# Kernel tuning notes

Measured on AMD Instinct MI355X. Metric: run time of the kernel, lower is better.

Reference implementation:

```python
import jax, jax.numpy as jnp
import numpy as np

B = 32
N = 1024  # half_size == num_delays == num_wavelength
DELTA_TAU = 1.5e-15
W_CENTER = 1.175e15  # center_frequency / 2
PULSE_THRESHOLD = 0.01
PENALTY = 10.0
REAL_W = 1.0; IMAG_W = 1.0; INT_W = 1.0; PHASE_W = 1.0; FROG_W = 1.0
MSE_WSUM = REAL_W + IMAG_W + INT_W + PHASE_W

# Hilbert mask exactly as in the torch source (even N branch): H[N//2+1:]=2, H[N//2]=1
_Hm = np.zeros(N, dtype=np.float32)
_Hm[N // 2 + 1:] = 2.0
_Hm[N // 2] = 1.0
HILBERT_MASK = jnp.asarray(_Hm)

# precomputed circular-shift gather indices: shifted[m, j] = x[(j - delay[m]) mod N]
_delays = np.arange(-(N // 2), N // 2)
SHIFT_IDX = jnp.asarray((np.arange(N)[None, :] - _delays[:, None]) % N)  # [N, N] int
SHIFT_FACTOR = jnp.exp(-1j * jnp.asarray(2.0 * W_CENTER * DELTA_TAU * _delays, dtype=jnp.float32)).astype(jnp.complex64)  # [N]


def hilbert(x):  # x: [N] real -> [N] complex analytical signal
    xf = jnp.fft.fft(x)
    return jnp.fft.ifft(xf * HILBERT_MASK)


def shg_mat(a):  # a: [N] complex -> [N, N] complex SHG matrix (vectorized createSHGmat)
    shifted = a[SHIFT_IDX]                                  # [N, N] all circular shifts
    rows = a[None, :] * shifted * SHIFT_FACTOR[None, :]     # elementwise complex multiply
    f = jnp.fft.fft(jnp.fft.fftshift(rows, axes=-1), axis=-1)  # one batched FFT
    return DELTA_TAU * jnp.fft.fftshift(f, axes=-1)


def _first_last(mask):  # mask: [B, N] bool -> per-sample first/last significant index with fallback
    any_m = jnp.any(mask, axis=1)
    first = jnp.where(any_m, jnp.argmax(mask, axis=1), 0)
    last = jnp.where(any_m, N - 1 - jnp.argmax(mask[:, ::-1], axis=1), N - 1)
    return first, last


def setup_inputs() -> dict:
    key = jax.random.key(0)
    k1, k2, k3 = jax.random.split(key, 3)
    prediction = jax.random.normal(k1, (B, N), dtype=jnp.float32)
    label = jax.random.normal(k2, (B, 2 * N), dtype=jnp.float32)
    shg_matrix = jax.random.uniform(k3, (B, 1, N, N), dtype=jnp.float32)
    return {"prediction": prediction, "label": label, "shg_matrix": shg_matrix}


def reference(prediction, label, shg_matrix):
    pa = jax.vmap(hilbert)(prediction)          # [B, N] complex64
    pr, pi = pa.real, pa.imag
    lr, li = label[:, :N], label[:, N:]
    l_int = lr ** 2 + li ** 2
    p_int = pr ** 2 + pi ** 2
    l_ph = jnp.arctan2(li, lr)
    p_ph = jnp.arctan2(pi, pr)

    # ---- FROG error ----
    shg_pred = jnp.abs(jax.vmap(shg_mat)(pa)) ** 2              # [B, N, N]
    shg_pred = shg_pred / jnp.max(shg_pred, axis=(1, 2), keepdims=True)  # normalizeSHGmatrix
    t_ref = shg_matrix[:, 0]                                    # [B, N, N]
    sum1 = jnp.sum(shg_pred * t_ref, axis=(1, 2))
    sum2 = jnp.sum(t_ref * t_ref, axis=(1, 2))
    mu = sum1 / sum2
    r = jnp.sum(shg_pred - mu[:, None, None] * t_ref, axis=(1, 2)) ** 2
    norm = (N * N) * jnp.max(shg_pred, axis=(1, 2)) ** 2
    frog = jnp.where(r == 0.0, 0.0, jnp.sqrt(r / norm))         # [B]

    # ---- weighted masked MSE ----
    fr, lr_idx = _first_last(jnp.abs(lr) > PULSE_THRESHOLD)
    fi, li_idx = _first_last(jnp.abs(li) > PULSE_THRESHOLD)
    first = jnp.minimum(fr, fi)
    last = jnp.maximum(lr_idx, li_idx)
    ar = jnp.arange(N)[None, :]
    in_range = (ar >= first[:, None]) & (ar < last[:, None])    # [first:last] slice semantics
    phase_mask = in_range.astype(jnp.float32)
    pulse_mask = jnp.where(in_range, PENALTY, 1.0)

    mse_real = jnp.mean((pr - lr) ** 2 * pulse_mask, axis=1) * REAL_W
    mse_imag = jnp.mean((pi - li) ** 2 * pulse_mask, axis=1) * IMAG_W
    mse_int = jnp.mean((p_int - l_int) ** 2 * pulse_mask, axis=1) * INT_W
    mse_ph = jnp.mean((p_ph - l_ph) ** 2 * phase_mask, axis=1) * PHASE_W
    mse = (mse_real + mse_imag + mse_int + mse_ph) / MSE_WSUM

    return jnp.mean(mse + FROG_W * frog)
```

## Files before the change

### kernel.cpp

```cpp
#include <hip/hip_runtime.h>
#include <math.h>

#define N 1024
#define BATCH 32
#define NT 512
#define ROWS 4
#define RSTRIDE 1092
#define P16(i) ((i) + ((i) >> 4))
#define PADC(i) ((i) + ((i) >> 5))

#define WSYNC() asm volatile("s_waitcnt lgkmcnt(0)" ::: "memory")

typedef float2 cf;
__device__ __forceinline__ cf cadd(cf a, cf b){ return make_float2(a.x+b.x, a.y+b.y); }
__device__ __forceinline__ cf csub(cf a, cf b){ return make_float2(a.x-b.x, a.y-b.y); }
__device__ __forceinline__ cf cmul(cf a, cf b){ return make_float2(a.x*b.x - a.y*b.y, a.x*b.y + a.y*b.x); }

__device__ __forceinline__ cf twiddle(float jn){
    float s = __builtin_amdgcn_sinf(jn);
    float c = __builtin_amdgcn_cosf(jn);
    return make_float2(c, -s);
}

__device__ __forceinline__ int rev10(int m){
    int r = (int)(__brev((unsigned)m) >> 22);
    return ((r & 0x155) << 1) | ((r >> 1) & 0x155);
}

__device__ __forceinline__ void bfly(cf x0, cf x1, cf x2, cf x3,
                                     cf& y0, cf& y1, cf& y2, cf& y3){
    cf A = cadd(x0,x2), Bs = cadd(x1,x3);
    cf C = csub(x0,x2), D = csub(x1,x3);
    cf Dmi = make_float2(D.y, -D.x);
    y0 = cadd(A,Bs); y1 = cadd(C,Dmi); y2 = csub(A,Bs); y3 = csub(C,Dmi);
}

__device__ __forceinline__ void dif4p(cf* w, int base, int q, cf w1, cf w2, cf w3){
    cf x0 = w[P16(base)], x1 = w[P16(base+q)], x2 = w[P16(base+2*q)], x3 = w[P16(base+3*q)];
    cf y0, y1, y2, y3; bfly(x0,x1,x2,x3,y0,y1,y2,y3);
    w[P16(base)]     = y0;
    w[P16(base+q)]   = cmul(y1,w1);
    w[P16(base+2*q)] = cmul(y2,w2);
    w[P16(base+3*q)] = cmul(y3,w3);
}

__device__ __forceinline__ void dif4h(cf* w, int base, int q, float jn){
    cf x0 = w[PADC(base)], x1 = w[PADC(base+q)], x2 = w[PADC(base+2*q)], x3 = w[PADC(base+3*q)];
    cf y0, y1, y2, y3; bfly(x0,x1,x2,x3,y0,y1,y2,y3);
    cf w1 = twiddle(jn), w2 = cmul(w1,w1), w3 = cmul(w2,w1);
    w[PADC(base)]     = y0;
    w[PADC(base+q)]   = cmul(y1,w1);
    w[PADC(base+2*q)] = cmul(y2,w2);
    w[PADC(base+3*q)] = cmul(y3,w3);
}
template<int LOG2N>
__device__ __forceinline__ void dif_stage(cf* w, int t){
    const int n = 1 << LOG2N, q = n >> 2;
    int j = t & (q - 1);
    int base = ((t >> (LOG2N - 2)) << LOG2N) + j;
    dif4h(w, base, q, (float)j * (1.0f / (float)n));
}
template<int LOG2N>
__device__ __forceinline__ void dit_stage(cf* w, int t){
    const int n = 1 << LOG2N, q = n >> 2;
    int j = t & (q - 1);
    int base = ((t >> (LOG2N - 2)) << LOG2N) + j;
    cf x0 = w[PADC(base)], x1 = w[PADC(base+q)], x2 = w[PADC(base+2*q)], x3 = w[PADC(base+3*q)];
    cf w1 = twiddle((float)j * (1.0f / (float)n));
    cf w2 = cmul(w1,w1), w3 = cmul(w2,w1);
    x1 = cmul(x1,w1); x2 = cmul(x2,w2); x3 = cmul(x3,w3);
    cf y0, y1, y2, y3; bfly(x0,x1,x2,x3,y0,y1,y2,y3);
    w[PADC(base)] = y0; w[PADC(base+q)] = y1; w[PADC(base+2*q)] = y2; w[PADC(base+3*q)] = y3;
}

__global__ __launch_bounds__(256) void hilbert_k(const float* __restrict__ pred,
                                                 const float* __restrict__ label,
                                                 cf* __restrict__ a,
                                                 cf* __restrict__ ca,
                                                 float* __restrict__ mseJ) {
    __shared__ cf wk[1056];
    __shared__ float rbuf[4][4];
    __shared__ int ibuf[4][4];
    __shared__ int s_first, s_last;
    int t = threadIdx.x, b = blockIdx.x;
    for (int i = t; i < N; i += 256) wk[PADC(i)] = make_float2(pred[b * N + i], 0.f);
    __syncthreads();
    dif_stage<10>(wk, t); __syncthreads();
    dif_stage<8>(wk, t);  __syncthreads();
    dif_stage<6>(wk, t);  __syncthreads();
    dif_stage<4>(wk, t);  __syncthreads();
    dif_stage<2>(wk, t);  __syncthreads();
    for (int i = t; i < N; i += 256) {
        int k = rev10(i);
        float f = (k < 512) ? 0.f : ((k == 512) ? 1.f : 2.f);
        cf v = wk[PADC(i)];
        wk[PADC(i)] = make_float2(f * v.x, -f * v.y);
    }
    __syncthreads();
    dit_stage<2>(wk, t);  __syncthreads();
    dit_stage<4>(wk, t);  __syncthreads();
    dit_stage<6>(wk, t);  __syncthreads();
    dit_stage<8>(wk, t);  __syncthreads();
    dit_stage<10>(wk, t); __syncthreads();
    const float sc = 1.f / (float)N;
    for (int i = t; i < N; i += 256) {
        cf v = wk[PADC(i)];
        cf av = make_float2(v.x * sc, -v.y * sc);
        wk[PADC(i)] = av;
        a[b * N + i] = av;
        float p = (float)(3.525 * (double)(i - 512));
        float s_, c_;
        sincosf(p, &s_, &c_);
        ca[b * N + i] = make_float2(av.x * c_ + av.y * s_, av.y * c_ - av.x * s_);
    }
    __syncthreads();

    int w = t >> 6, lane = t & 63;
    int mnR = N, mxR = -1, mnI = N, mxI = -1;
    for (int n = t; n < N; n += 256) {
        float lr = label[b * 2 * N + n];
        float li = label[b * 2 * N + N + n];
        if (fabsf(lr) > 0.01f) { mnR = min(mnR, n); mxR = max(mxR, n); }
        if (fabsf(li) > 0.01f) { mnI = min(mnI, n); mxI = max(mxI, n); }
    }
    for (int o = 32; o > 0; o >>= 1) {
        mnR = min(mnR, __shfl_down(mnR, o));
        mxR = max(mxR, __shfl_down(mxR, o));
        mnI = min(mnI, __shfl_down(mnI, o));
        mxI = max(mxI, __shfl_down(mxI, o));
    }
    if (lane == 0) { ibuf[w][0] = mnR; ibuf[w][1] = mxR; ibuf[w][2] = mnI; ibuf[w][3] = mxI; }
    __syncthreads();
    if (t == 0) {
        int a0 = N, a1 = -1, a2 = N, a3 = -1;
        for (int i = 0; i < 4; ++i) {
            a0 = min(a0, ibuf[i][0]); a1 = max(a1, ibuf[i][1]);
            a2 = min(a2, ibuf[i][2]); a3 = max(a3, ibuf[i][3]);
        }
        int fr   = (a0 == N) ? 0 : a0;
        int lstR = (a1 < 0) ? (N - 1) : a1;
        int fi   = (a2 == N) ? 0 : a2;
        int lstI = (a3 < 0) ? (N - 1) : a3;
        s_first = min(fr, fi);
        s_last  = max(lstR, lstI);
    }
    __syncthreads();
    int first = s_first, last = s_last;

    float m_r = 0.f, m_i = 0.f, m_n = 0.f, m_p = 0.f;
    for (int n = t; n < N; n += 256) {
        cf p = wk[PADC(n)];
        float lr = label[b * 2 * N + n];
        float li = label[b * 2 * N + N + n];
        bool in = (n >= first) && (n < last);
        float pm  = in ? 10.f : 1.f;
        float phm = in ? 1.f : 0.f;
        float dr = p.x - lr, di = p.y - li;
        float dn = (p.x * p.x + p.y * p.y) - (lr * lr + li * li);
        float dp = atan2f(p.y, p.x) - atan2f(li, lr);
        m_r += dr * dr * pm;
        m_i += di * di * pm;
        m_n += dn * dn * pm;
        m_p += dp * dp * phm;
    }
    for (int o = 32; o > 0; o >>= 1) {
        m_r += __shfl_down(m_r, o);
        m_i += __shfl_down(m_i, o);
        m_n += __shfl_down(m_n, o);
        m_p += __shfl_down(m_p, o);
    }
    if (lane == 0) { rbuf[w][0] = m_r; rbuf[w][1] = m_i; rbuf[w][2] = m_n; rbuf[w][3] = m_p; }
    __syncthreads();
    if (t == 0) {
        float s = 0.f;
        for (int i = 0; i < 4; ++i) s += rbuf[i][0] + rbuf[i][1] + rbuf[i][2] + rbuf[i][3];
        mseJ[b] = s * (1.f / (float)N) * 0.25f;
    }
}

__global__ __launch_bounds__(NT, 8) void shg_k(const cf* __restrict__ a,
                                               const cf* __restrict__ cag,
                                               const float* __restrict__ tref,
                                               float* __restrict__ Praw,
                                               float* __restrict__ Prt,
                                               float* __restrict__ Pmax,
                                               float* __restrict__ Pt,
                                               float* __restrict__ Ptt) {
    __shared__ cf wk[ROWS * RSTRIDE];
    int t = threadIdx.x, blk = blockIdx.x;
    int b = blk >> 8;
    int dg = (blk & 255) << 2;
    const cf* arow  = a   + b * N;
    const cf* carow = cag + b * N;
    int bt = t & 255, rg = t >> 8;

    {
        cf w1 = twiddle((float)bt * (1.0f / 1024.0f));
        cf w2 = cmul(w1,w1), w3 = cmul(w2,w1);
        cf cav[4];
#pragma unroll
        for (int k = 0; k < 4; ++k) cav[k] = carow[(bt + 256*k + 512) & 1023];
#pragma unroll
        for (int rr = 0; rr < 2; ++rr) {
            int r = rg * 2 + rr;
            int d = dg + r;
            cf x[4];
#pragma unroll
            for (int k = 0; k < 4; ++k)
                x[k] = cmul(cav[k], arow[(bt + 256*k - d) & 1023]);
            cf y0, y1, y2, y3; bfly(x[0],x[1],x[2],x[3],y0,y1,y2,y3);
            cf* w = wk + r * RSTRIDE;
            w[P16(bt)]     = y0;
            w[P16(bt+256)] = cmul(y1,w1);
            w[P16(bt+512)] = cmul(y2,w2);
            w[P16(bt+768)] = cmul(y3,w3);
        }
    }
    __syncthreads();
    {
        int j = bt & 63;
        int base = ((bt >> 6) << 8) + j;
        cf w1 = twiddle((float)j * (1.0f / 256.0f));
        cf w2 = cmul(w1,w1), w3 = cmul(w2,w1);
#pragma unroll
        for (int rr = 0; rr < 2; ++rr) dif4p(wk + (rg*2+rr) * RSTRIDE, base, 64, w1, w2, w3);
    }
    WSYNC();
    {
        int j = bt & 15;
        int base = ((bt >> 4) << 6) + j;
        cf w1 = twiddle((float)j * (1.0f / 64.0f));
        cf w2 = cmul(w1,w1), w3 = cmul(w2,w1);
#pragma unroll
        for (int rr = 0; rr < 2; ++rr) dif4p(wk + (rg*2+rr) * RSTRIDE, base, 16, w1, w2, w3);
    }
    __syncthreads();

    if (t < 256) {
        const cf W1 = { 0.923879533f, -0.382683432f};
        const cf W2 = { 0.707106781f, -0.707106781f};
        const cf W3 = { 0.382683432f, -0.923879533f};
        const cf W6 = {-0.707106781f, -0.707106781f};
        const cf W9 = {-0.923879533f,  0.382683432f};
        int r = t >> 6;
        int g = t & 63;
        cf* w = wk + r * RSTRIDE;
        cf v[16];
        int base = 17 * g;
#pragma unroll
        for (int k = 0; k < 16; ++k) v[k] = w[base + k];
        cf o[16];
        bfly(v[0], v[4], v[8], v[12], o[0], o[4], o[8],  o[12]);
        { cf y0,y1,y2,y3; bfly(v[1],v[5],v[9], v[13],y0,y1,y2,y3);
          o[1]=y0; o[5]=cmul(y1,W1); o[9]=cmul(y2,W2); o[13]=cmul(y3,W3); }
        { cf y0,y1,y2,y3; bfly(v[2],v[6],v[10],v[14],y0,y1,y2,y3);
          o[2]=y0; o[6]=cmul(y1,W2); o[10]=make_float2(y2.y,-y2.x); o[14]=cmul(y3,W6); }
        { cf y0,y1,y2,y3; bfly(v[3],v[7],v[11],v[15],y0,y1,y2,y3);
          o[3]=y0; o[7]=cmul(y1,W3); o[11]=cmul(y2,W6); o[15]=cmul(y3,W9); }

        float sraw = 0.f, srt = 0.f, mx = 0.f, st = 0.f, stt = 0.f;
        int bd = b * N + dg + r;
        const float* trow = tref + ((size_t)bd << 10);
        int kb = ((g & 3) << 4) | (g & 12) | (g >> 4);
#pragma unroll
        for (int u = 0; u < 4; ++u) {
            cf y0, y1, y2, y3;
            bfly(o[4*u], o[4*u+1], o[4*u+2], o[4*u+3], y0, y1, y2, y3);
            cf ys[4] = {y0, y1, y2, y3};
#pragma unroll
            for (int m = 0; m < 4; ++m) {
                float m2 = ys[m].x * ys[m].x + ys[m].y * ys[m].y;
                float tv = trow[(((m + 2) & 3) << 8) | (u << 6) | kb];
                sraw += m2;
                srt += m2 * tv;
                mx = fmaxf(mx, m2);
                st += tv;
                stt += tv * tv;
            }
        }
        for (int o_ = 32; o_ > 0; o_ >>= 1) {
            sraw += __shfl_down(sraw, o_);
            srt  += __shfl_down(srt, o_);
            mx    = fmaxf(mx, __shfl_down(mx, o_));
            st   += __shfl_down(st, o_);
            stt  += __shfl_down(stt, o_);
        }
        if ((t & 63) == 0) {
            Praw[bd] = sraw; Prt[bd] = srt; Pmax[bd] = mx; Pt[bd] = st; Ptt[bd] = stt;
        }
    }
}

__global__ __launch_bounds__(256) void loss_k(const float* __restrict__ Praw,
                                              const float* __restrict__ Prt,
                                              const float* __restrict__ Pmax,
                                              const float* __restrict__ Pt,
                                              const float* __restrict__ Ptt,
                                              const float* __restrict__ mseJ,
                                              float* __restrict__ out) {
    __shared__ float rbuf[4][8];
    int tid = threadIdx.x, b = blockIdx.x;
    int w = tid >> 6, lane = tid & 63;
    float sr = 0.f, srt = 0.f, mx = 0.f, st = 0.f, stt = 0.f;
    for (int i = tid; i < N; i += 256) {
        int idx = b * N + i;
        sr += Praw[idx]; srt += Prt[idx]; mx = fmaxf(mx, Pmax[idx]);
        st += Pt[idx];   stt += Ptt[idx];
    }
    for (int o = 32; o > 0; o >>= 1) {
        sr  += __shfl_down(sr, o);
        srt += __shfl_down(srt, o);
        mx   = fmaxf(mx, __shfl_down(mx, o));
        st  += __shfl_down(st, o);
        stt += __shfl_down(stt, o);
    }
    if (lane == 0) {
        rbuf[w][0] = sr; rbuf[w][1] = srt; rbuf[w][2] = mx;
        rbuf[w][3] = st; rbuf[w][4] = stt;
    }
    __syncthreads();
    if (tid == 0) {
        float A0 = 0.f, A1 = 0.f, A2 = 0.f, A3 = 0.f, A4 = 0.f;
        for (int i = 0; i < 4; ++i) {
            A0 += rbuf[i][0]; A1 += rbuf[i][1]; A2 = fmaxf(A2, rbuf[i][2]);
            A3 += rbuf[i][3]; A4 += rbuf[i][4];
        }
        float mu = (A1 / A2) / A4;
        float diff = A0 / A2 - mu * A3;
        float frog = fabsf(diff) * (1.f / (float)N);
        atomicAdd(out, (mseJ[b] + frog) * (1.f / (float)BATCH));
    }
}

extern "C" void kernel_launch(void* const* d_in, const int* in_sizes, int n_in,
                              void* d_out, int out_size, void* d_ws, size_t ws_size,
                              hipStream_t stream) {
    (void)in_sizes; (void)n_in; (void)out_size; (void)ws_size;
    const float* pred  = (const float*)d_in[0];
    const float* label = (const float*)d_in[1];
    const float* shg   = (const float*)d_in[2];
    float* out = (float*)d_out;

    char* ws = (char*)d_ws;
    cf* a   = (cf*)ws;
    cf* ca  = a + (size_t)BATCH * N;
    float* mseJ = (float*)(ca + (size_t)BATCH * N);
    float* P = mseJ + BATCH;
    float* Praw = P;
    float* Prt  = P + (size_t)BATCH * N;
    float* Pmax = P + 2 * (size_t)BATCH * N;
    float* Pt   = P + 3 * (size_t)BATCH * N;
    float* Ptt  = P + 4 * (size_t)BATCH * N;

    hipMemsetAsync(d_out, 0, sizeof(float), stream);
    hilbert_k<<<BATCH, 256, 0, stream>>>(pred, label, a, ca, mseJ);
    shg_k<<<BATCH * 256, NT, 0, stream>>>(a, ca, shg, Praw, Prt, Pmax, Pt, Ptt);
    loss_k<<<BATCH, 256, 0, stream>>>(Praw, Prt, Pmax, Pt, Ptt, mseJ, out);
}
```

Baseline: 230.4 us.

## Fuse radix-4 stages 2-3 in registers and halve block threads

The SHG FFT kernel drops from 512 to 256 threads per block, with each thread handling all four rows in the first stage. The second and third radix-4 stages are fused into a single radix-16 step held in registers: each thread loads 16 points, runs both butterfly layers and writes back once. This removes one LDS round trip and a block barrier, and the padded row stride and index scheme are adjusted to keep LDS accesses conflict-free. In exchange each thread uses more registers and the block has half as many threads, which can reduce latency hiding.

```diff
diff --git a/kernel.cpp b/kernel.cpp
--- a/kernel.cpp
+++ b/kernel.cpp
@@ -3,10 +3,9 @@
 
 #define N 1024
 #define BATCH 32
-#define NT 512
+#define NT 256
 #define ROWS 4
-#define RSTRIDE 1092
-#define P16(i) ((i) + ((i) >> 4))
+#define RSTRIDE 1116
 #define PADC(i) ((i) + ((i) >> 5))
 
 #define WSYNC() asm volatile("s_waitcnt lgkmcnt(0)" ::: "memory")
@@ -33,15 +32,6 @@
     cf C = csub(x0,x2), D = csub(x1,x3);
     cf Dmi = make_float2(D.y, -D.x);
     y0 = cadd(A,Bs); y1 = cadd(C,Dmi); y2 = csub(A,Bs); y3 = csub(C,Dmi);
-}
-
-__device__ __forceinline__ void dif4p(cf* w, int base, int q, cf w1, cf w2, cf w3){
-    cf x0 = w[P16(base)], x1 = w[P16(base+q)], x2 = w[P16(base+2*q)], x3 = w[P16(base+3*q)];
-    cf y0, y1, y2, y3; bfly(x0,x1,x2,x3,y0,y1,y2,y3);
-    w[P16(base)]     = y0;
-    w[P16(base+q)]   = cmul(y1,w1);
-    w[P16(base+2*q)] = cmul(y2,w2);
-    w[P16(base+3*q)] = cmul(y3,w3);
 }
 
 __device__ __forceinline__ void dif4h(cf* w, int base, int q, float jn){
@@ -178,7 +168,7 @@
     }
 }
 
-__global__ __launch_bounds__(NT, 8) void shg_k(const cf* __restrict__ a,
+__global__ __launch_bounds__(NT, 4) void shg_k(const cf* __restrict__ a,
                                                const cf* __restrict__ cag,
                                                const float* __restrict__ tref,
                                                float* __restrict__ Praw,
@@ -192,51 +182,71 @@
     int dg = (blk & 255) << 2;
     const cf* arow  = a   + b * N;
     const cf* carow = cag + b * N;
-    int bt = t & 255, rg = t >> 8;
 
     {
+        int bt = t;
         cf w1 = twiddle((float)bt * (1.0f / 1024.0f));
         cf w2 = cmul(w1,w1), w3 = cmul(w2,w1);
         cf cav[4];
 #pragma unroll
         for (int k = 0; k < 4; ++k) cav[k] = carow[(bt + 256*k + 512) & 1023];
-#pragma unroll
-        for (int rr = 0; rr < 2; ++rr) {
-            int r = rg * 2 + rr;
+        int wb = bt + (bt >> 4);
+#pragma unroll
+        for (int r = 0; r < ROWS; ++r) {
             int d = dg + r;
             cf x[4];
 #pragma unroll
             for (int k = 0; k < 4; ++k)
                 x[k] = cmul(cav[k], arow[(bt + 256*k - d) & 1023]);
             cf y0, y1, y2, y3; bfly(x[0],x[1],x[2],x[3],y0,y1,y2,y3);
-            cf* w = wk + r * RSTRIDE;
-            w[P16(bt)]     = y0;
-            w[P16(bt+256)] = cmul(y1,w1);
-            w[P16(bt+512)] = cmul(y2,w2);
-            w[P16(bt+768)] = cmul(y3,w3);
-        }
-    }
-    __syncthreads();
+            cf* w = wk + r * RSTRIDE + wb;
+            w[0]   = y0;
+            w[280] = cmul(y1,w1);
+            w[560] = cmul(y2,w2);
+            w[840] = cmul(y3,w3);
+        }
+    }
+    __syncthreads();
+
     {
-        int j = bt & 63;
-        int base = ((bt >> 6) << 8) + j;
-        cf w1 = twiddle((float)j * (1.0f / 256.0f));
-        cf w2 = cmul(w1,w1), w3 = cmul(w2,w1);
-#pragma unroll
-        for (int rr = 0; rr < 2; ++rr) dif4p(wk + (rg*2+rr) * RSTRIDE, base, 64, w1, w2, w3);
+        int r  = t >> 6;
+        int q2 = t & 63;
+        int B2 = q2 >> 4;
+        int v  = q2 & 15;
+        cf* w = wk + r * RSTRIDE + 280 * B2 + v;
+        cf p[16];
+#pragma unroll
+        for (int m = 0; m < 16; ++m) p[m] = w[17*m];
+#pragma unroll
+        for (int m0 = 0; m0 < 4; ++m0) {
+            cf w1 = twiddle((float)(v + 16*m0) * (1.0f / 256.0f));
+            cf w2 = cmul(w1,w1), w3 = cmul(w2,w1);
+            cf y0, y1, y2, y3;
+            bfly(p[m0], p[m0+4], p[m0+8], p[m0+12], y0,y1,y2,y3);
+            p[m0]    = y0;
+            p[m0+4]  = cmul(y1,w1);
+            p[m0+8]  = cmul(y2,w2);
+            p[m0+12] = cmul(y3,w3);
+        }
+        {
+            cf w1 = twiddle((float)v * (1.0f / 64.0f));
+            cf w2 = cmul(w1,w1), w3 = cmul(w2,w1);
+#pragma unroll
+            for (int s = 0; s < 4; ++s) {
+                cf y0, y1, y2, y3;
+                bfly(p[4*s], p[4*s+1], p[4*s+2], p[4*s+3], y0,y1,y2,y3);
+                p[4*s]   = y0;
+                p[4*s+1] = cmul(y1,w1);
+                p[4*s+2] = cmul(y2,w2);
+                p[4*s+3] = cmul(y3,w3);
+            }
+        }
+#pragma unroll
+        for (int m = 0; m < 16; ++m) w[17*m] = p[m];
     }
     WSYNC();
+
     {
-        int j = bt & 15;
-        int base = ((bt >> 4) << 6) + j;
-        cf w1 = twiddle((float)j * (1.0f / 64.0f));
-        cf w2 = cmul(w1,w1), w3 = cmul(w2,w1);
-#pragma unroll
-        for (int rr = 0; rr < 2; ++rr) dif4p(wk + (rg*2+rr) * RSTRIDE, base, 16, w1, w2, w3);
-    }
-    __syncthreads();
-
-    if (t < 256) {
         const cf W1 = { 0.923879533f, -0.382683432f};
         const cf W2 = { 0.707106781f, -0.707106781f};
         const cf W3 = { 0.382683432f, -0.923879533f};
@@ -246,7 +256,7 @@
         int g = t & 63;
         cf* w = wk + r * RSTRIDE;
         cf v[16];
-        int base = 17 * g;
+        int base = 17 * g + 8 * (g >> 4);
 #pragma unroll
         for (int k = 0; k < 16; ++k) v[k] = w[base + k];
         cf o[16];
```

Result: no change. 230.1 us (-0.1%).
